# Kernel optimization log

Hardware: AMD Instinct MI355X
Metric: run time of the kernel (lower is better)

The kernel has to match this reference:

```python
import jax, jax.numpy as jnp
import numpy as np

N_NODES = 20000
N_EDGES = 200000
D_IN = 32      # nf_input_dim
D_H = 32       # nf_hide_dim
D_OUT = 8      # nf_output_dim
E_DIM = 16     # edge_dim


def setup_inputs() -> dict:
    key = jax.random.key(0)
    ks = jax.random.split(key, 20)
    s = 0.1
    inp = {
        "x": jax.random.normal(ks[0], (N_NODES, D_IN), jnp.float32),
        "edge_attr": jax.random.normal(ks[1], (N_EDGES, E_DIM), jnp.float32),
        "edge_index": jax.random.randint(ks[2], (2, N_EDGES), 0, N_NODES, jnp.int32),
    }
    # layer 0: edge MLP (E_DIM->E_DIM->D_IN*D_H), root [D_IN,D_H], bias [D_H]
    inp["w1_0"] = jax.random.normal(ks[3], (E_DIM, E_DIM), jnp.float32) * s
    inp["b1_0"] = jnp.zeros((E_DIM,), jnp.float32)
    inp["w2_0"] = jax.random.normal(ks[4], (E_DIM, D_IN * D_H), jnp.float32) * s
    inp["b2_0"] = jnp.zeros((D_IN * D_H,), jnp.float32)
    inp["root_0"] = jax.random.normal(ks[5], (D_IN, D_H), jnp.float32) * s
    inp["bias_0"] = jnp.zeros((D_H,), jnp.float32)
    # layer 1: edge MLP (E_DIM->E_DIM->D_H*D_H), root [D_H,D_H], bias [D_H]
    inp["w1_1"] = jax.random.normal(ks[6], (E_DIM, E_DIM), jnp.float32) * s
    inp["b1_1"] = jnp.zeros((E_DIM,), jnp.float32)
    inp["w2_1"] = jax.random.normal(ks[7], (E_DIM, D_H * D_H), jnp.float32) * s
    inp["b2_1"] = jnp.zeros((D_H * D_H,), jnp.float32)
    inp["root_1"] = jax.random.normal(ks[8], (D_H, D_H), jnp.float32) * s
    inp["bias_1"] = jnp.zeros((D_H,), jnp.float32)
    # classifier
    inp["cls_w"] = jax.random.normal(ks[9], (D_H, D_OUT), jnp.float32) * s
    inp["cls_b"] = jnp.zeros((D_OUT,), jnp.float32)
    return inp


def _nnconv(x, edge_attr, src, dst, inv_count, w1, b1, w2, b2, root, bias, din, dout, n):
    # edge network: Linear -> ELU -> Linear producing per-edge weight matrix [E, din, dout]
    h = jax.nn.elu(edge_attr @ w1 + b1)
    theta = (h @ w2 + b2).reshape(-1, din, dout)
    # gather source features, per-edge matvec, scatter-mean into dst
    msg = jnp.einsum("ei,eio->eo", x[src], theta)          # [E, dout]
    agg = jax.ops.segment_sum(msg, dst, num_segments=n) * inv_count[:, None]
    return agg + x @ root + bias                            # root weight + bias (PyG defaults)


def reference(x, edge_attr, edge_index,
              w1_0, b1_0, w2_0, b2_0, root_0, bias_0,
              w1_1, b1_1, w2_1, b2_1, root_1, bias_1,
              cls_w, cls_b):
    n = x.shape[0]
    src, dst = edge_index[0], edge_index[1]
    deg = jax.ops.segment_sum(jnp.ones(src.shape[0], x.dtype), dst, num_segments=n)
    inv_count = 1.0 / jnp.maximum(deg, 1.0)
    h = jax.nn.elu(_nnconv(x, edge_attr, src, dst, inv_count,
                           w1_0, b1_0, w2_0, b2_0, root_0, bias_0, D_IN, D_H, n))
    h = jax.nn.elu(_nnconv(h, edge_attr, src, dst, inv_count,
                           w1_1, b1_1, w2_1, b2_1, root_1, bias_1, D_H, D_H, n))
    # dropout is identity in eval mode
    return h @ cls_w + cls_b
```

## Files before the change

### kernel.cpp

```cpp
#include <hip/hip_runtime.h>
#include <hip/hip_bf16.h>
#include <math.h>

#define N_NODES 20000
#define N_EDGES 200000
#define D_H 32
#define E_DIM 16
#define CAP 40
#define NJOBS1 (N_EDGES / 16)
#define GBASE1 ((NJOBS1 + 7) / 8)
#define ABASE (N_NODES / 4)
#define W2S_SHORTS (17 * 2 * 64 * 8)
#define PREP_SHORTS (W2S_SHORTS + 512)
#define XPAIRS (N_NODES * 16)
#define EAPAIRS (N_EDGES * 8)
#define IB2 1563

typedef __attribute__((ext_vector_type(8))) short bf16x8;
typedef __attribute__((ext_vector_type(4))) float f32x4;

__device__ __forceinline__ float elu_f(float v) { return v > 0.f ? v : expm1f(v); }
__device__ __forceinline__ short f2bf(float f) {
    union { __hip_bfloat16 h; short s; } u;
    u.h = __float2bfloat16(f);
    return u.s;
}
__device__ __forceinline__ float bf2f(__hip_bfloat16 h) { return __bfloat162float(h); }
__device__ __forceinline__ unsigned pack2(float lo, float hi) {
    return (unsigned)(unsigned short)f2bf(lo) | ((unsigned)(unsigned short)f2bf(hi) << 16);
}

__global__ __launch_bounds__(256)
void init_kernel(const float* __restrict__ w2_0, const float* __restrict__ b2_0,
                 const float* __restrict__ w1_0, const float* __restrict__ b1_0,
                 const float* __restrict__ w2_1, const float* __restrict__ b2_1,
                 const float* __restrict__ w1_1, const float* __restrict__ b1_1,
                 const float* __restrict__ x, const float* __restrict__ ea,
                 int* __restrict__ cnt, short* __restrict__ prep,
                 unsigned* __restrict__ xbf, unsigned* __restrict__ eabf)
{
    const int gid = blockIdx.x * 256 + threadIdx.x;
    const int nth = IB2 * 256;
    if (gid < N_NODES) cnt[gid] = 0;
    if (gid < 2 * PREP_SHORTS) {
        int layer = gid >= PREP_SHORTS ? 1 : 0;
        int r = gid - layer * PREP_SHORTS;
        const float* w2 = layer ? w2_1 : w2_0;
        const float* b2 = layer ? b2_1 : b2_0;
        const float* w1 = layer ? w1_1 : w1_0;
        const float* b1 = layer ? b1_1 : b1_0;
        float v;
        if (r < W2S_SHORTS) {
            int j = r & 7, l = (r >> 3) & 63, ct = (r >> 9) & 1, kk = r >> 10;
            int ii = (l >> 4) * 8 + j;
            int o = ct * 16 + (l & 15);
            v = (kk < 16) ? w2[kk * 1024 + ii * 32 + o] : b2[ii * 32 + o];
        } else {
            int q = r - W2S_SHORTS;
            int j = q & 7, l = q >> 3;
            int m = l & 15, k = (l >> 4) * 8 + j;
            v = (k < 16) ? w1[k * 16 + m] : (k == 16 ? b1[m] : 0.f);
        }
        prep[gid] = f2bf(v);
    }
    for (int i = gid; i < XPAIRS; i += nth) {
        const float2 p = *(const float2*)(x + (size_t)i * 2);
        xbf[i] = pack2(p.x, p.y);
    }
    for (int i = gid; i < EAPAIRS; i += nth) {
        const float2 p = *(const float2*)(ea + (size_t)i * 2);
        eabf[i] = pack2(p.x, p.y);
    }
}

__global__ __launch_bounds__(256)
void hist_kernel(const int* __restrict__ dst, int* __restrict__ cnt, int* __restrict__ ord) {
    int e = blockIdx.x * 256 + threadIdx.x;
    if (e < N_EDGES) ord[e] = atomicAdd(&cnt[dst[e]], 1);
}

__global__ __launch_bounds__(1024)
void scan_kernel(const int* __restrict__ cnt, int* __restrict__ rowptr) {
    __shared__ int part[1024];
    const int t = threadIdx.x;
    const int base = t * 20;
    int loc[20];
    int sum = 0;
    #pragma unroll
    for (int j = 0; j < 20; ++j) {
        int idx = base + j;
        int v = (idx < N_NODES) ? cnt[idx] : 0;
        loc[j] = v;
        sum += v;
    }
    part[t] = sum;
    __syncthreads();
    for (int off = 1; off < 1024; off <<= 1) {
        int v = (t >= off) ? part[t - off] : 0;
        __syncthreads();
        part[t] += v;
        __syncthreads();
    }
    int run = part[t] - sum;
    #pragma unroll
    for (int j = 0; j < 20; ++j) {
        int idx = base + j;
        if (idx < N_NODES) { rowptr[idx] = run; run += loc[j]; }
    }
    if (t == 0) rowptr[N_NODES] = N_EDGES;
}

template<int MODE>
__global__ __launch_bounds__(512)
void edge_kernel(const short* __restrict__ xbf,
                 const short* __restrict__ eabf,
                 const int* __restrict__ src,
                 const int* __restrict__ dst,
                 int* __restrict__ cnt,
                 int* __restrict__ pebuf,
                 const int* __restrict__ ord,
                 const int* __restrict__ rowptr,
                 const short* __restrict__ prepL,
                 __hip_bfloat16* __restrict__ msg)
{
    __shared__ __align__(16) short w2s[PREP_SHORTS];

    const int t = threadIdx.x;
    for (int i = t; i < PREP_SHORTS / 8; i += 512)
        ((int4*)w2s)[i] = ((const int4*)prepL)[i];
    __syncthreads();

    const int lane = t & 63;
    const int wave = t >> 6;
    const int job = blockIdx.x * 8 + wave;
    if (job >= NJOBS1) return;
    const int eloc = lane & 15;
    const int kg = lane >> 4;

    const int e0 = job * 16 + eloc;

    int pe0;
    if (MODE == 0) {
        int p0_ = 0;
        if (kg == 0) {
            const int d0 = dst[e0];
            p0_ = d0 * CAP + atomicAdd(&cnt[d0], 1);
            pebuf[e0] = p0_;
        }
        pe0 = __shfl(p0_, eloc);
    } else if (MODE == 1) {
        pe0 = pebuf[e0];
    } else {
        pe0 = rowptr[dst[e0]] + ord[e0];
    }

    const int sn0 = src[e0];

    bf16x8 xf0 = *(const bf16x8*)(xbf + (size_t)sn0 * 32 + kg * 8);

    bf16x8 ea0 = {0,0,0,0,0,0,0,0};
    if (kg < 2) {
        ea0 = *(const bf16x8*)(eabf + (size_t)e0 * E_DIM + kg * 8);
    } else if (kg == 2) {
        ea0[0] = f2bf(1.0f);
    }

    const f32x4 zero4 = {0.f, 0.f, 0.f, 0.f};

    bf16x8 w1f = *(const bf16x8*)&w2s[W2S_SHORTS + lane * 8];
    f32x4 hd0 = __builtin_amdgcn_mfma_f32_16x16x32_bf16(w1f, ea0, zero4, 0, 0, 0);
    float hv0[4];
    #pragma unroll
    for (int r = 0; r < 4; ++r) hv0[r] = elu_f(hd0[r]);

    float m00[4]={0,0,0,0}, m01[4]={0,0,0,0};
    #pragma unroll
    for (int kk = 0; kk < 17; ++kk) {
        bf16x8 a0 = *(const bf16x8*)&w2s[(kk * 2 + 0) * 512 + lane * 8];
        bf16x8 a1 = *(const bf16x8*)&w2s[(kk * 2 + 1) * 512 + lane * 8];
        float h0;
        if (kk < 16) {
            h0 = __shfl(hv0[kk & 3], (kk >> 2) * 16 + eloc);
        } else {
            h0 = 1.0f;
        }
        f32x4 d00 = __builtin_amdgcn_mfma_f32_16x16x32_bf16(a0, xf0, zero4, 0, 0, 0);
        f32x4 d01 = __builtin_amdgcn_mfma_f32_16x16x32_bf16(a1, xf0, zero4, 0, 0, 0);
        #pragma unroll
        for (int r = 0; r < 4; ++r) {
            m00[r] += h0 * d00[r];
            m01[r] += h0 * d01[r];
        }
    }

    short* mp0 = (short*)(msg + (size_t)pe0 * D_H);
    short q00[4] = { f2bf(m00[0]), f2bf(m00[1]), f2bf(m00[2]), f2bf(m00[3]) };
    short q01[4] = { f2bf(m01[0]), f2bf(m01[1]), f2bf(m01[2]), f2bf(m01[3]) };
    *(int2*)(mp0 + kg * 4)      = *(int2*)q00;
    *(int2*)(mp0 + 16 + kg * 4) = *(int2*)q01;
}

template<bool LAST, bool PADDED>
__global__ __launch_bounds__(256)
void agg_kernel(const void* __restrict__ xin_,
                const __hip_bfloat16* __restrict__ msg,
                const int* __restrict__ rowptr,
                const int* __restrict__ cnt,
                const float* __restrict__ root,
                const float* __restrict__ bias,
                const float* __restrict__ cls_w,
                const float* __restrict__ cls_b,
                __hip_bfloat16* __restrict__ hout,
                float* __restrict__ out)
{
    __shared__ float root_s[32 * 32];
    __shared__ float bias_s[32];
    __shared__ float h2_s[4][33];
    const int t = threadIdx.x;
    for (int i = t; i < 1024; i += 256) root_s[i] = root[i];
    if (t < 32) bias_s[t] = bias[t];
    __syncthreads();

    const int lane = t & 63;
    const int wave = t >> 6;
    const int o = lane & 31;
    const int half = lane >> 5;
    const int n = blockIdx.x * 4 + wave;

    int start, end;
    if (PADDED) { start = n * CAP; end = start + cnt[n]; }
    else        { start = rowptr[n]; end = rowptr[n + 1]; }

    float s = 0.f;
    int j = start + half;
    for (; j + 6 < end; j += 8) {
        float v0 = bf2f(msg[(size_t)(j    ) * D_H + o]);
        float v1 = bf2f(msg[(size_t)(j + 2) * D_H + o]);
        float v2 = bf2f(msg[(size_t)(j + 4) * D_H + o]);
        float v3 = bf2f(msg[(size_t)(j + 6) * D_H + o]);
        s += (v0 + v1) + (v2 + v3);
    }
    for (; j < end; j += 2)
        s += bf2f(msg[(size_t)j * D_H + o]);
    s += __shfl_xor(s, 32);

    float acc = s * (1.f / fmaxf((float)(end - start), 1.f)) + bias_s[o];
    const float xv = LAST ? bf2f(((const __hip_bfloat16*)xin_)[(size_t)n * 32 + o])
                          : ((const float*)xin_)[(size_t)n * 32 + o];
    #pragma unroll
    for (int i = 0; i < 32; ++i)
        acc += __shfl(xv, half * 32 + i) * root_s[i * 32 + o];
    acc = elu_f(acc);

    if (!LAST) {
        if (half == 0) hout[(size_t)n * 32 + o] = __float2bfloat16(acc);
    } else {
        if (half == 0) h2_s[wave][o] = acc;
        __syncthreads();
        if (t < 32) {
            const int nn = t >> 3, jj = t & 7;
            float a = cls_b[jj];
            #pragma unroll
            for (int i = 0; i < 32; ++i) a += h2_s[nn][i] * cls_w[i * 8 + jj];
            out[(size_t)(blockIdx.x * 4 + nn) * 8 + jj] = a;
        }
    }
}

extern "C" void kernel_launch(void* const* d_in, const int* in_sizes, int n_in,
                              void* d_out, int out_size, void* d_ws, size_t ws_size,
                              hipStream_t stream)
{
    const float* x          = (const float*)d_in[0];
    const float* edge_attr  = (const float*)d_in[1];
    const int*   edge_index = (const int*)d_in[2];
    const float* w1_0 = (const float*)d_in[3];
    const float* b1_0 = (const float*)d_in[4];
    const float* w2_0 = (const float*)d_in[5];
    const float* b2_0 = (const float*)d_in[6];
    const float* root_0 = (const float*)d_in[7];
    const float* bias_0 = (const float*)d_in[8];
    const float* w1_1 = (const float*)d_in[9];
    const float* b1_1 = (const float*)d_in[10];
    const float* w2_1 = (const float*)d_in[11];
    const float* b2_1 = (const float*)d_in[12];
    const float* root_1 = (const float*)d_in[13];
    const float* bias_1 = (const float*)d_in[14];
    const float* cls_w = (const float*)d_in[15];
    const float* cls_b = (const float*)d_in[16];

    const int* src = edge_index;
    const int* dst = edge_index + N_EDGES;

    const int EB = (N_EDGES + 255) / 256;

    size_t need = 0;
    size_t o_cnt = need;  need += (size_t)N_NODES * 4;
    size_t o_pe  = need;  need += (size_t)N_EDGES * 4;
    size_t o_prep= (need + 15) & ~(size_t)15; need = o_prep + (size_t)2 * PREP_SHORTS * 2;
    size_t o_xbf = (need + 15) & ~(size_t)15; need = o_xbf + (size_t)N_NODES * 32 * 2;
    size_t o_ea  = (need + 15) & ~(size_t)15; need = o_ea  + (size_t)N_EDGES * 16 * 2;
    size_t o_msg = (need + 63) & ~(size_t)63; need = o_msg + (size_t)N_NODES * CAP * D_H * 2;
    size_t o_hb  = (need + 15) & ~(size_t)15; need = o_hb + (size_t)N_NODES * D_H * 2;

    char* ws = (char*)d_ws;

    if (ws_size >= need) {
        int* cnt = (int*)(ws + o_cnt);
        int* pe  = (int*)(ws + o_pe);
        short* prep = (short*)(ws + o_prep);
        unsigned* xbf  = (unsigned*)(ws + o_xbf);
        unsigned* eabf = (unsigned*)(ws + o_ea);
        __hip_bfloat16* msg  = (__hip_bfloat16*)(ws + o_msg);
        __hip_bfloat16* hbuf = (__hip_bfloat16*)(ws + o_hb);

        init_kernel<<<IB2, 256, 0, stream>>>(w2_0, b2_0, w1_0, b1_0,
                                             w2_1, b2_1, w1_1, b1_1,
                                             x, edge_attr, cnt, prep, xbf, eabf);
        edge_kernel<0><<<GBASE1, 512, 0, stream>>>((const short*)xbf, (const short*)eabf,
                                                   src, dst, cnt, pe, nullptr, nullptr,
                                                   prep, msg);
        agg_kernel<false, true><<<ABASE, 256, 0, stream>>>(x, msg, nullptr, cnt,
                                                           root_0, bias_0, nullptr, nullptr,
                                                           hbuf, nullptr);
        edge_kernel<1><<<GBASE1, 512, 0, stream>>>((const short*)hbuf, (const short*)eabf,
                                                   src, dst, nullptr, pe, nullptr, nullptr,
                                                   prep + PREP_SHORTS, msg);
        agg_kernel<true, true><<<ABASE, 256, 0, stream>>>(hbuf, msg, nullptr, cnt,
                                                          root_1, bias_1, cls_w, cls_b,
                                                          nullptr, (float*)d_out);
    } else {
        size_t f = 0;
        int* cnt    = (int*)ws;                 f += (size_t)N_NODES * 4;
        int* rowptr = (int*)(ws + f);           f += (size_t)(N_NODES + 1) * 4;
        int* ord    = (int*)(ws + f);           f += (size_t)N_EDGES * 4;
        f = (f + 15) & ~(size_t)15;
        short* prep = (short*)(ws + f);         f += (size_t)2 * PREP_SHORTS * 2;
        f = (f + 15) & ~(size_t)15;
        unsigned* xbf = (unsigned*)(ws + f);    f += (size_t)N_NODES * 32 * 2;
        f = (f + 15) & ~(size_t)15;
        unsigned* eabf = (unsigned*)(ws + f);   f += (size_t)N_EDGES * 16 * 2;
        f = (f + 63) & ~(size_t)63;
        __hip_bfloat16* msg = (__hip_bfloat16*)(ws + f); f += (size_t)N_EDGES * D_H * 2;
        f = (f + 15) & ~(size_t)15;
        __hip_bfloat16* hbuf = (__hip_bfloat16*)(ws + f);

        init_kernel<<<IB2, 256, 0, stream>>>(w2_0, b2_0, w1_0, b1_0,
                                             w2_1, b2_1, w1_1, b1_1,
                                             x, edge_attr, cnt, prep, xbf, eabf);
        hist_kernel<<<EB, 256, 0, stream>>>(dst, cnt, ord);
        scan_kernel<<<1, 1024, 0, stream>>>(cnt, rowptr);

        edge_kernel<2><<<GBASE1, 512, 0, stream>>>((const short*)xbf, (const short*)eabf,
                                                   src, dst, nullptr, nullptr, ord, rowptr,
                                                   prep, msg);
        agg_kernel<false, false><<<ABASE, 256, 0, stream>>>(x, msg, rowptr, nullptr,
                                                            root_0, bias_0, nullptr, nullptr,
                                                            hbuf, nullptr);
        edge_kernel<2><<<GBASE1, 512, 0, stream>>>((const short*)hbuf, (const short*)eabf,
                                                   src, dst, nullptr, nullptr, ord, rowptr,
                                                   prep + PREP_SHORTS, msg);
        agg_kernel<true, false><<<ABASE, 256, 0, stream>>>(hbuf, msg, rowptr, nullptr,
                                                           root_1, bias_1, cls_w, cls_b,
                                                           nullptr, (float*)d_out);
    }
}
```

Before: 80.17 us.

## Fuse edge message and node aggregation into one dst-sorted layer kernel

```diff
diff --git a/kernel.cpp b/kernel.cpp
--- a/kernel.cpp
+++ b/kernel.cpp
@@ -7,9 +7,8 @@
 #define D_H 32
 #define E_DIM 16
 #define CAP 40
-#define NJOBS1 (N_EDGES / 16)
-#define GBASE1 ((NJOBS1 + 7) / 8)
-#define ABASE (N_NODES / 4)
+#define NPB 16
+#define LGRID (N_NODES / NPB)
 #define W2S_SHORTS (17 * 2 * 64 * 8)
 #define PREP_SHORTS (W2S_SHORTS + 512)
 #define XPAIRS (N_NODES * 16)
@@ -74,195 +73,149 @@
 }
 
 __global__ __launch_bounds__(256)
-void hist_kernel(const int* __restrict__ dst, int* __restrict__ cnt, int* __restrict__ ord) {
+void fill_kernel(const int* __restrict__ dst, int* __restrict__ cnt, int* __restrict__ elist) {
     int e = blockIdx.x * 256 + threadIdx.x;
-    if (e < N_EDGES) ord[e] = atomicAdd(&cnt[dst[e]], 1);
-}
-
-__global__ __launch_bounds__(1024)
-void scan_kernel(const int* __restrict__ cnt, int* __restrict__ rowptr) {
-    __shared__ int part[1024];
-    const int t = threadIdx.x;
-    const int base = t * 20;
-    int loc[20];
-    int sum = 0;
-    #pragma unroll
-    for (int j = 0; j < 20; ++j) {
-        int idx = base + j;
-        int v = (idx < N_NODES) ? cnt[idx] : 0;
-        loc[j] = v;
-        sum += v;
-    }
-    part[t] = sum;
-    __syncthreads();
-    for (int off = 1; off < 1024; off <<= 1) {
-        int v = (t >= off) ? part[t - off] : 0;
-        __syncthreads();
-        part[t] += v;
-        __syncthreads();
-    }
-    int run = part[t] - sum;
-    #pragma unroll
-    for (int j = 0; j < 20; ++j) {
-        int idx = base + j;
-        if (idx < N_NODES) { rowptr[idx] = run; run += loc[j]; }
-    }
-    if (t == 0) rowptr[N_NODES] = N_EDGES;
-}
-
-template<int MODE>
+    if (e < N_EDGES) {
+        int d = dst[e];
+        int r = atomicAdd(&cnt[d], 1);
+        elist[d * CAP + r] = e;
+    }
+}
+
+template<bool LAST>
 __global__ __launch_bounds__(512)
-void edge_kernel(const short* __restrict__ xbf,
-                 const short* __restrict__ eabf,
-                 const int* __restrict__ src,
-                 const int* __restrict__ dst,
-                 int* __restrict__ cnt,
-                 int* __restrict__ pebuf,
-                 const int* __restrict__ ord,
-                 const int* __restrict__ rowptr,
-                 const short* __restrict__ prepL,
-                 __hip_bfloat16* __restrict__ msg)
+void layer_kernel(const short* __restrict__ xin,
+                  const short* __restrict__ eabf,
+                  const int* __restrict__ src,
+                  const int* __restrict__ elist,
+                  const int* __restrict__ cnt,
+                  const short* __restrict__ prepL,
+                  const float* __restrict__ root,
+                  const float* __restrict__ bias,
+                  const float* __restrict__ cls_w,
+                  const float* __restrict__ cls_b,
+                  __hip_bfloat16* __restrict__ hout,
+                  float* __restrict__ out)
 {
     __shared__ __align__(16) short w2s[PREP_SHORTS];
+    __shared__ float root_s[1024];
+    __shared__ float bias_s[32];
+    __shared__ float acc[NPB + 1][32];
+    __shared__ int   list[NPB * CAP];
+    __shared__ int   off_s[NPB + 1];
+    __shared__ float h2_s[LAST ? NPB : 1][33];
 
     const int t = threadIdx.x;
+    const int nb = blockIdx.x * NPB;
+
     for (int i = t; i < PREP_SHORTS / 8; i += 512)
         ((int4*)w2s)[i] = ((const int4*)prepL)[i];
+    for (int i = t; i < 1024; i += 512) root_s[i] = root[i];
+    if (t < 32) bias_s[t] = bias[t];
+    for (int i = t; i < (NPB + 1) * 32; i += 512) ((float*)acc)[i] = 0.f;
+    if (t == 0) {
+        int run = 0;
+        #pragma unroll
+        for (int ln = 0; ln < NPB; ++ln) { off_s[ln] = run; run += cnt[nb + ln]; }
+        off_s[NPB] = run;
+    }
+    __syncthreads();
+
+    {
+        const int ln = t >> 5;
+        const int j0 = t & 31;
+        const int c = cnt[nb + ln];
+        const int base = off_s[ln];
+        for (int j = j0; j < c; j += 32)
+            list[base + j] = (ln << 20) | elist[(nb + ln) * CAP + j];
+    }
     __syncthreads();
 
     const int lane = t & 63;
     const int wave = t >> 6;
-    const int job = blockIdx.x * 8 + wave;
-    if (job >= NJOBS1) return;
     const int eloc = lane & 15;
     const int kg = lane >> 4;
-
-    const int e0 = job * 16 + eloc;
-
-    int pe0;
-    if (MODE == 0) {
-        int p0_ = 0;
-        if (kg == 0) {
-            const int d0 = dst[e0];
-            p0_ = d0 * CAP + atomicAdd(&cnt[d0], 1);
-            pebuf[e0] = p0_;
-        }
-        pe0 = __shfl(p0_, eloc);
-    } else if (MODE == 1) {
-        pe0 = pebuf[e0];
-    } else {
-        pe0 = rowptr[dst[e0]] + ord[e0];
-    }
-
-    const int sn0 = src[e0];
-
-    bf16x8 xf0 = *(const bf16x8*)(xbf + (size_t)sn0 * 32 + kg * 8);
-
-    bf16x8 ea0 = {0,0,0,0,0,0,0,0};
-    if (kg < 2) {
-        ea0 = *(const bf16x8*)(eabf + (size_t)e0 * E_DIM + kg * 8);
-    } else if (kg == 2) {
-        ea0[0] = f2bf(1.0f);
-    }
-
+    const int total = off_s[NPB];
+    const int ntiles = (total + 15) / 16;
     const f32x4 zero4 = {0.f, 0.f, 0.f, 0.f};
-
-    bf16x8 w1f = *(const bf16x8*)&w2s[W2S_SHORTS + lane * 8];
-    f32x4 hd0 = __builtin_amdgcn_mfma_f32_16x16x32_bf16(w1f, ea0, zero4, 0, 0, 0);
-    float hv0[4];
-    #pragma unroll
-    for (int r = 0; r < 4; ++r) hv0[r] = elu_f(hd0[r]);
-
-    float m00[4]={0,0,0,0}, m01[4]={0,0,0,0};
-    #pragma unroll
-    for (int kk = 0; kk < 17; ++kk) {
-        bf16x8 a0 = *(const bf16x8*)&w2s[(kk * 2 + 0) * 512 + lane * 8];
-        bf16x8 a1 = *(const bf16x8*)&w2s[(kk * 2 + 1) * 512 + lane * 8];
-        float h0;
-        if (kk < 16) {
-            h0 = __shfl(hv0[kk & 3], (kk >> 2) * 16 + eloc);
+    const bf16x8 w1f = *(const bf16x8*)&w2s[W2S_SHORTS + lane * 8];
+
+    for (int tile = wave; tile < ntiles; tile += 8) {
+        const int slot = tile * 16 + eloc;
+        const int packed = (slot < total) ? list[slot] : (NPB << 20);
+        const int ln = packed >> 20;
+        const int e0 = packed & 0xFFFFF;
+
+        const int sn0 = src[e0];
+        const bf16x8 xf0 = *(const bf16x8*)(xin + (size_t)sn0 * 32 + kg * 8);
+
+        bf16x8 ea0 = {0, 0, 0, 0, 0, 0, 0, 0};
+        if (kg < 2) {
+            ea0 = *(const bf16x8*)(eabf + (size_t)e0 * E_DIM + kg * 8);
+        } else if (kg == 2) {
+            ea0[0] = f2bf(1.0f);
+        }
+
+        f32x4 hd0 = __builtin_amdgcn_mfma_f32_16x16x32_bf16(w1f, ea0, zero4, 0, 0, 0);
+        float hv0[4];
+        #pragma unroll
+        for (int r = 0; r < 4; ++r) hv0[r] = elu_f(hd0[r]);
+
+        float m00[4] = {0, 0, 0, 0}, m01[4] = {0, 0, 0, 0};
+        #pragma unroll
+        for (int kk = 0; kk < 17; ++kk) {
+            bf16x8 a0 = *(const bf16x8*)&w2s[(kk * 2 + 0) * 512 + lane * 8];
+            bf16x8 a1 = *(const bf16x8*)&w2s[(kk * 2 + 1) * 512 + lane * 8];
+            float h0;
+            if (kk < 16) {
+                h0 = __shfl(hv0[kk & 3], (kk >> 2) * 16 + eloc);
+            } else {
+                h0 = 1.0f;
+            }
+            f32x4 d00 = __builtin_amdgcn_mfma_f32_16x16x32_bf16(a0, xf0, zero4, 0, 0, 0);
+            f32x4 d01 = __builtin_amdgcn_mfma_f32_16x16x32_bf16(a1, xf0, zero4, 0, 0, 0);
+            #pragma unroll
+            for (int r = 0; r < 4; ++r) {
+                m00[r] += h0 * d00[r];
+                m01[r] += h0 * d01[r];
+            }
+        }
+
+        float* arow = acc[ln];
+        #pragma unroll
+        for (int r = 0; r < 4; ++r) {
+            atomicAdd(&arow[kg * 4 + r],      m00[r]);
+            atomicAdd(&arow[16 + kg * 4 + r], m01[r]);
+        }
+    }
+    __syncthreads();
+
+    {
+        const int half = lane >> 5;
+        const int o = lane & 31;
+        const int ln = wave * 2 + half;
+        const int n = nb + ln;
+        const int c = cnt[n];
+
+        float a = acc[ln][o] * (1.f / fmaxf((float)c, 1.f)) + bias_s[o];
+        const float xv = bf2f(((const __hip_bfloat16*)xin)[(size_t)n * 32 + o]);
+        #pragma unroll
+        for (int i = 0; i < 32; ++i)
+            a += __shfl(xv, half * 32 + i) * root_s[i * 32 + o];
+        a = elu_f(a);
+
+        if (!LAST) {
+            hout[(size_t)n * 32 + o] = __float2bfloat16(a);
         } else {
-            h0 = 1.0f;
-        }
-        f32x4 d00 = __builtin_amdgcn_mfma_f32_16x16x32_bf16(a0, xf0, zero4, 0, 0, 0);
-        f32x4 d01 = __builtin_amdgcn_mfma_f32_16x16x32_bf16(a1, xf0, zero4, 0, 0, 0);
-        #pragma unroll
-        for (int r = 0; r < 4; ++r) {
-            m00[r] += h0 * d00[r];
-            m01[r] += h0 * d01[r];
-        }
-    }
-
-    short* mp0 = (short*)(msg + (size_t)pe0 * D_H);
-    short q00[4] = { f2bf(m00[0]), f2bf(m00[1]), f2bf(m00[2]), f2bf(m00[3]) };
-    short q01[4] = { f2bf(m01[0]), f2bf(m01[1]), f2bf(m01[2]), f2bf(m01[3]) };
-    *(int2*)(mp0 + kg * 4)      = *(int2*)q00;
-    *(int2*)(mp0 + 16 + kg * 4) = *(int2*)q01;
-}
-
-template<bool LAST, bool PADDED>
-__global__ __launch_bounds__(256)
-void agg_kernel(const void* __restrict__ xin_,
-                const __hip_bfloat16* __restrict__ msg,
-                const int* __restrict__ rowptr,
-                const int* __restrict__ cnt,
-                const float* __restrict__ root,
-                const float* __restrict__ bias,
-                const float* __restrict__ cls_w,
-                const float* __restrict__ cls_b,
-                __hip_bfloat16* __restrict__ hout,
-                float* __restrict__ out)
-{
-    __shared__ float root_s[32 * 32];
-    __shared__ float bias_s[32];
-    __shared__ float h2_s[4][33];
-    const int t = threadIdx.x;
-    for (int i = t; i < 1024; i += 256) root_s[i] = root[i];
-    if (t < 32) bias_s[t] = bias[t];
-    __syncthreads();
-
-    const int lane = t & 63;
-    const int wave = t >> 6;
-    const int o = lane & 31;
-    const int half = lane >> 5;
-    const int n = blockIdx.x * 4 + wave;
-
-    int start, end;
-    if (PADDED) { start = n * CAP; end = start + cnt[n]; }
-    else        { start = rowptr[n]; end = rowptr[n + 1]; }
-
-    float s = 0.f;
-    int j = start + half;
-    for (; j + 6 < end; j += 8) {
-        float v0 = bf2f(msg[(size_t)(j    ) * D_H + o]);
-        float v1 = bf2f(msg[(size_t)(j + 2) * D_H + o]);
-        float v2 = bf2f(msg[(size_t)(j + 4) * D_H + o]);
-        float v3 = bf2f(msg[(size_t)(j + 6) * D_H + o]);
-        s += (v0 + v1) + (v2 + v3);
-    }
-    for (; j < end; j += 2)
-        s += bf2f(msg[(size_t)j * D_H + o]);
-    s += __shfl_xor(s, 32);
-
-    float acc = s * (1.f / fmaxf((float)(end - start), 1.f)) + bias_s[o];
-    const float xv = LAST ? bf2f(((const __hip_bfloat16*)xin_)[(size_t)n * 32 + o])
-                          : ((const float*)xin_)[(size_t)n * 32 + o];
-    #pragma unroll
-    for (int i = 0; i < 32; ++i)
-        acc += __shfl(xv, half * 32 + i) * root_s[i * 32 + o];
-    acc = elu_f(acc);
-
-    if (!LAST) {
-        if (half == 0) hout[(size_t)n * 32 + o] = __float2bfloat16(acc);
-    } else {
-        if (half == 0) h2_s[wave][o] = acc;
-        __syncthreads();
-        if (t < 32) {
-            const int nn = t >> 3, jj = t & 7;
-            float a = cls_b[jj];
-            #pragma unroll
-            for (int i = 0; i < 32; ++i) a += h2_s[nn][i] * cls_w[i * 8 + jj];
-            out[(size_t)(blockIdx.x * 4 + nn) * 8 + jj] = a;
+            h2_s[ln][o] = a;
+            __syncthreads();
+            if (t < NPB * 8) {
+                const int nn = t >> 3, jj = t & 7;
+                float s = cls_b[jj];
+                #pragma unroll
+                for (int i = 0; i < 32; ++i) s += h2_s[nn][i] * cls_w[i * 8 + jj];
+                out[(size_t)(nb + nn) * 8 + jj] = s;
+            }
         }
     }
 }
@@ -294,74 +247,28 @@
 
     const int EB = (N_EDGES + 255) / 256;
 
-    size_t need = 0;
-    size_t o_cnt = need;  need += (size_t)N_NODES * 4;
-    size_t o_pe  = need;  need += (size_t)N_EDGES * 4;
-    size_t o_prep= (need + 15) & ~(size_t)15; need = o_prep + (size_t)2 * PREP_SHORTS * 2;
-    size_t o_xbf = (need + 15) & ~(size_t)15; need = o_xbf + (size_t)N_NODES * 32 * 2;
-    size_t o_ea  = (need + 15) & ~(size_t)15; need = o_ea  + (size_t)N_EDGES * 16 * 2;
-    size_t o_msg = (need + 63) & ~(size_t)63; need = o_msg + (size_t)N_NODES * CAP * D_H * 2;
-    size_t o_hb  = (need + 15) & ~(size_t)15; need = o_hb + (size_t)N_NODES * D_H * 2;
-
-    char* ws = (char*)d_ws;
-
-    if (ws_size >= need) {
-        int* cnt = (int*)(ws + o_cnt);
-        int* pe  = (int*)(ws + o_pe);
-        short* prep = (short*)(ws + o_prep);
-        unsigned* xbf  = (unsigned*)(ws + o_xbf);
-        unsigned* eabf = (unsigned*)(ws + o_ea);
-        __hip_bfloat16* msg  = (__hip_bfloat16*)(ws + o_msg);
-        __hip_bfloat16* hbuf = (__hip_bfloat16*)(ws + o_hb);
-
-        init_kernel<<<IB2, 256, 0, stream>>>(w2_0, b2_0, w1_0, b1_0,
-                                             w2_1, b2_1, w1_1, b1_1,
-                                             x, edge_attr, cnt, prep, xbf, eabf);
-        edge_kernel<0><<<GBASE1, 512, 0, stream>>>((const short*)xbf, (const short*)eabf,
-                                                   src, dst, cnt, pe, nullptr, nullptr,
-                                                   prep, msg);
-        agg_kernel<false, true><<<ABASE, 256, 0, stream>>>(x, msg, nullptr, cnt,
-                                                           root_0, bias_0, nullptr, nullptr,
-                                                           hbuf, nullptr);
-        edge_kernel<1><<<GBASE1, 512, 0, stream>>>((const short*)hbuf, (const short*)eabf,
-                                                   src, dst, nullptr, pe, nullptr, nullptr,
-                                                   prep + PREP_SHORTS, msg);
-        agg_kernel<true, true><<<ABASE, 256, 0, stream>>>(hbuf, msg, nullptr, cnt,
-                                                          root_1, bias_1, cls_w, cls_b,
-                                                          nullptr, (float*)d_out);
-    } else {
-        size_t f = 0;
-        int* cnt    = (int*)ws;                 f += (size_t)N_NODES * 4;
-        int* rowptr = (int*)(ws + f);           f += (size_t)(N_NODES + 1) * 4;
-        int* ord    = (int*)(ws + f);           f += (size_t)N_EDGES * 4;
-        f = (f + 15) & ~(size_t)15;
-        short* prep = (short*)(ws + f);         f += (size_t)2 * PREP_SHORTS * 2;
-        f = (f + 15) & ~(size_t)15;
-        unsigned* xbf = (unsigned*)(ws + f);    f += (size_t)N_NODES * 32 * 2;
-        f = (f + 15) & ~(size_t)15;
-        unsigned* eabf = (unsigned*)(ws + f);   f += (size_t)N_EDGES * 16 * 2;
-        f = (f + 63) & ~(size_t)63;
-        __hip_bfloat16* msg = (__hip_bfloat16*)(ws + f); f += (size_t)N_EDGES * D_H * 2;
-        f = (f + 15) & ~(size_t)15;
-        __hip_bfloat16* hbuf = (__hip_bfloat16*)(ws + f);
-
-        init_kernel<<<IB2, 256, 0, stream>>>(w2_0, b2_0, w1_0, b1_0,
-                                             w2_1, b2_1, w1_1, b1_1,
-                                             x, edge_attr, cnt, prep, xbf, eabf);
-        hist_kernel<<<EB, 256, 0, stream>>>(dst, cnt, ord);
-        scan_kernel<<<1, 1024, 0, stream>>>(cnt, rowptr);
-
-        edge_kernel<2><<<GBASE1, 512, 0, stream>>>((const short*)xbf, (const short*)eabf,
-                                                   src, dst, nullptr, nullptr, ord, rowptr,
-                                                   prep, msg);
-        agg_kernel<false, false><<<ABASE, 256, 0, stream>>>(x, msg, rowptr, nullptr,
-                                                            root_0, bias_0, nullptr, nullptr,
-                                                            hbuf, nullptr);
-        edge_kernel<2><<<GBASE1, 512, 0, stream>>>((const short*)hbuf, (const short*)eabf,
-                                                   src, dst, nullptr, nullptr, ord, rowptr,
-                                                   prep + PREP_SHORTS, msg);
-        agg_kernel<true, false><<<ABASE, 256, 0, stream>>>(hbuf, msg, rowptr, nullptr,
-                                                           root_1, bias_1, cls_w, cls_b,
-                                                           nullptr, (float*)d_out);
-    }
-}
+    size_t off = 0;
+    int* cnt = (int*)((char*)d_ws + off);            off += (size_t)N_NODES * 4;
+    int* elist = (int*)((char*)d_ws + off);          off += (size_t)N_NODES * CAP * 4;
+    off = (off + 15) & ~(size_t)15;
+    short* prep = (short*)((char*)d_ws + off);       off += (size_t)2 * PREP_SHORTS * 2;
+    off = (off + 15) & ~(size_t)15;
+    unsigned* xbf = (unsigned*)((char*)d_ws + off);  off += (size_t)N_NODES * 32 * 2;
+    off = (off + 15) & ~(size_t)15;
+    unsigned* eabf = (unsigned*)((char*)d_ws + off); off += (size_t)N_EDGES * 16 * 2;
+    off = (off + 15) & ~(size_t)15;
+    __hip_bfloat16* hbuf = (__hip_bfloat16*)((char*)d_ws + off);
+
+    init_kernel<<<IB2, 256, 0, stream>>>(w2_0, b2_0, w1_0, b1_0,
+                                         w2_1, b2_1, w1_1, b1_1,
+                                         x, edge_attr, cnt, prep, xbf, eabf);
+    fill_kernel<<<EB, 256, 0, stream>>>(dst, cnt, elist);
+    layer_kernel<false><<<LGRID, 512, 0, stream>>>((const short*)xbf, (const short*)eabf,
+                                                   src, elist, cnt, prep,
+                                                   root_0, bias_0, nullptr, nullptr,
+                                                   hbuf, nullptr);
+    layer_kernel<true><<<LGRID, 512, 0, stream>>>((const short*)hbuf, (const short*)eabf,
+                                                  src, elist, cnt, prep + PREP_SHORTS,
+                                                  root_1, bias_1, cls_w, cls_b,
+                                                  nullptr, (float*)d_out);
+}
```

After: 184.2 us. +129.8%, slower.

## Switch edge kernel to 32x32x16 MFMA with 32 edges per wave

Applied to the files above, without the earlier changes.

```diff
diff --git a/kernel.cpp b/kernel.cpp
--- a/kernel.cpp
+++ b/kernel.cpp
@@ -7,17 +7,20 @@
 #define D_H 32
 #define E_DIM 16
 #define CAP 40
-#define NJOBS1 (N_EDGES / 16)
-#define GBASE1 ((NJOBS1 + 7) / 8)
+#define NJOBS32 (N_EDGES / 32)
+#define GB32 ((NJOBS32 + 7) / 8)
 #define ABASE (N_NODES / 4)
 #define W2S_SHORTS (17 * 2 * 64 * 8)
-#define PREP_SHORTS (W2S_SHORTS + 512)
+#define W1_OFF W2S_SHORTS
+#define B1_OFF (W2S_SHORTS + 512)
+#define PREP_SHORTS (W2S_SHORTS + 512 + 32)
 #define XPAIRS (N_NODES * 16)
 #define EAPAIRS (N_EDGES * 8)
 #define IB2 1563
 
 typedef __attribute__((ext_vector_type(8))) short bf16x8;
 typedef __attribute__((ext_vector_type(4))) float f32x4;
+typedef __attribute__((ext_vector_type(16))) float f32x16;
 
 __device__ __forceinline__ float elu_f(float v) { return v > 0.f ? v : expm1f(v); }
 __device__ __forceinline__ short f2bf(float f) {
@@ -26,6 +29,11 @@
     return u.s;
 }
 __device__ __forceinline__ float bf2f(__hip_bfloat16 h) { return __bfloat162float(h); }
+__device__ __forceinline__ float bfbits2f(short s) {
+    union { __hip_bfloat16 h; short s; } u;
+    u.s = s;
+    return __bfloat162float(u.h);
+}
 __device__ __forceinline__ unsigned pack2(float lo, float hi) {
     return (unsigned)(unsigned short)f2bf(lo) | ((unsigned)(unsigned short)f2bf(hi) << 16);
 }
@@ -51,15 +59,18 @@
         const float* b1 = layer ? b1_1 : b1_0;
         float v;
         if (r < W2S_SHORTS) {
-            int j = r & 7, l = (r >> 3) & 63, ct = (r >> 9) & 1, kk = r >> 10;
-            int ii = (l >> 4) * 8 + j;
-            int o = ct * 16 + (l & 15);
-            v = (kk < 16) ? w2[kk * 1024 + ii * 32 + o] : b2[ii * 32 + o];
+            int j = r & 7, l = (r >> 3) & 63, half = (r >> 9) & 1, kk = r >> 10;
+            int i = half * 16 + ((l >> 5) << 3) + j;
+            int o = l & 31;
+            v = (kk < 16) ? w2[kk * 1024 + i * 32 + o] : b2[i * 32 + o];
+        } else if (r < B1_OFF) {
+            int q = r - W1_OFF;
+            int j = q & 7, l = q >> 3;
+            int ko = l & 31, ki = ((l >> 5) << 3) + j;
+            v = (ko < 16) ? w1[ki * 16 + ko] : 0.f;
         } else {
-            int q = r - W2S_SHORTS;
-            int j = q & 7, l = q >> 3;
-            int m = l & 15, k = (l >> 4) * 8 + j;
-            v = (k < 16) ? w1[k * 16 + m] : (k == 16 ? b1[m] : 0.f);
+            int j = r - B1_OFF;
+            v = (j < 16) ? b1[j] : 0.f;
         }
         prep[gid] = f2bf(v);
     }
@@ -133,71 +144,74 @@
     const int lane = t & 63;
     const int wave = t >> 6;
     const int job = blockIdx.x * 8 + wave;
-    if (job >= NJOBS1) return;
-    const int eloc = lane & 15;
-    const int kg = lane >> 4;
-
-    const int e0 = job * 16 + eloc;
-
-    int pe0;
+    if (job >= NJOBS32) return;
+    const int ec = lane & 31;
+    const int hl = lane >> 5;
+
+    const int e = job * 32 + ec;
+
+    int pe;
     if (MODE == 0) {
-        int p0_ = 0;
-        if (kg == 0) {
-            const int d0 = dst[e0];
-            p0_ = d0 * CAP + atomicAdd(&cnt[d0], 1);
-            pebuf[e0] = p0_;
+        int p_ = 0;
+        if (hl == 0) {
+            const int d = dst[e];
+            p_ = d * CAP + atomicAdd(&cnt[d], 1);
+            pebuf[e] = p_;
         }
-        pe0 = __shfl(p0_, eloc);
+        pe = __shfl(p_, ec);
     } else if (MODE == 1) {
-        pe0 = pebuf[e0];
+        pe = pebuf[e];
     } else {
-        pe0 = rowptr[dst[e0]] + ord[e0];
-    }
-
-    const int sn0 = src[e0];
-
-    bf16x8 xf0 = *(const bf16x8*)(xbf + (size_t)sn0 * 32 + kg * 8);
-
-    bf16x8 ea0 = {0,0,0,0,0,0,0,0};
-    if (kg < 2) {
-        ea0 = *(const bf16x8*)(eabf + (size_t)e0 * E_DIM + kg * 8);
-    } else if (kg == 2) {
-        ea0[0] = f2bf(1.0f);
-    }
-
-    const f32x4 zero4 = {0.f, 0.f, 0.f, 0.f};
-
-    bf16x8 w1f = *(const bf16x8*)&w2s[W2S_SHORTS + lane * 8];
-    f32x4 hd0 = __builtin_amdgcn_mfma_f32_16x16x32_bf16(w1f, ea0, zero4, 0, 0, 0);
-    float hv0[4];
-    #pragma unroll
-    for (int r = 0; r < 4; ++r) hv0[r] = elu_f(hd0[r]);
-
-    float m00[4]={0,0,0,0}, m01[4]={0,0,0,0};
+        pe = rowptr[dst[e]] + ord[e];
+    }
+
+    const int sn = src[e];
+
+    const bf16x8 xb0 = *(const bf16x8*)(xbf + (size_t)sn * 32 + hl * 8);
+    const bf16x8 xb1 = *(const bf16x8*)(xbf + (size_t)sn * 32 + 16 + hl * 8);
+
+    const bf16x8 eaB = *(const bf16x8*)(eabf + (size_t)e * E_DIM + hl * 8);
+
+    const f32x16 zero16 = {0.f,0.f,0.f,0.f,0.f,0.f,0.f,0.f,0.f,0.f,0.f,0.f,0.f,0.f,0.f,0.f};
+
+    const bf16x8 w1A = *(const bf16x8*)&w2s[W1_OFF + lane * 8];
+    f32x16 hd = __builtin_amdgcn_mfma_f32_32x32x16_bf16(w1A, eaB, zero16, 0, 0, 0);
+    float hv[8];
+    #pragma unroll
+    for (int r = 0; r < 8; ++r) {
+        const int row = (r & 3) + 8 * (r >> 2) + 4 * hl;
+        hv[r] = elu_f(hd[r] + bfbits2f(w2s[B1_OFF + row]));
+    }
+
+    float mr[16];
+    #pragma unroll
+    for (int r = 0; r < 16; ++r) mr[r] = 0.f;
+
     #pragma unroll
     for (int kk = 0; kk < 17; ++kk) {
-        bf16x8 a0 = *(const bf16x8*)&w2s[(kk * 2 + 0) * 512 + lane * 8];
-        bf16x8 a1 = *(const bf16x8*)&w2s[(kk * 2 + 1) * 512 + lane * 8];
-        float h0;
+        const bf16x8 a0 = *(const bf16x8*)&w2s[((kk * 2 + 0) * 64 + lane) * 8];
+        const bf16x8 a1 = *(const bf16x8*)&w2s[((kk * 2 + 1) * 64 + lane) * 8];
+        f32x16 d = __builtin_amdgcn_mfma_f32_32x32x16_bf16(a0, xb0, zero16, 0, 0, 0);
+        d = __builtin_amdgcn_mfma_f32_32x32x16_bf16(a1, xb1, d, 0, 0, 0);
+        float h;
         if (kk < 16) {
-            h0 = __shfl(hv0[kk & 3], (kk >> 2) * 16 + eloc);
+            const int hlk = (kk >> 2) & 1;
+            const int rk = (kk & 3) | ((kk & 8) >> 1);
+            h = __shfl(hv[rk], hlk * 32 + ec);
         } else {
-            h0 = 1.0f;
+            h = 1.0f;
         }
-        f32x4 d00 = __builtin_amdgcn_mfma_f32_16x16x32_bf16(a0, xf0, zero4, 0, 0, 0);
-        f32x4 d01 = __builtin_amdgcn_mfma_f32_16x16x32_bf16(a1, xf0, zero4, 0, 0, 0);
         #pragma unroll
-        for (int r = 0; r < 4; ++r) {
-            m00[r] += h0 * d00[r];
-            m01[r] += h0 * d01[r];
-        }
-    }
-
-    short* mp0 = (short*)(msg + (size_t)pe0 * D_H);
-    short q00[4] = { f2bf(m00[0]), f2bf(m00[1]), f2bf(m00[2]), f2bf(m00[3]) };
-    short q01[4] = { f2bf(m01[0]), f2bf(m01[1]), f2bf(m01[2]), f2bf(m01[3]) };
-    *(int2*)(mp0 + kg * 4)      = *(int2*)q00;
-    *(int2*)(mp0 + 16 + kg * 4) = *(int2*)q01;
+        for (int r = 0; r < 16; ++r) mr[r] += h * d[r];
+    }
+
+    short* mp = (short*)(msg + (size_t)pe * D_H);
+    #pragma unroll
+    for (int g = 0; g < 4; ++g) {
+        short q[4] = { f2bf(mr[g * 4 + 0]), f2bf(mr[g * 4 + 1]),
+                       f2bf(mr[g * 4 + 2]), f2bf(mr[g * 4 + 3]) };
+        *(int2*)(mp + 8 * g + 4 * hl) = *(int2*)q;
+    }
 }
 
 template<bool LAST, bool PADDED>
@@ -317,15 +331,15 @@
         init_kernel<<<IB2, 256, 0, stream>>>(w2_0, b2_0, w1_0, b1_0,
                                              w2_1, b2_1, w1_1, b1_1,
                                              x, edge_attr, cnt, prep, xbf, eabf);
-        edge_kernel<0><<<GBASE1, 512, 0, stream>>>((const short*)xbf, (const short*)eabf,
-                                                   src, dst, cnt, pe, nullptr, nullptr,
-                                                   prep, msg);
+        edge_kernel<0><<<GB32, 512, 0, stream>>>((const short*)xbf, (const short*)eabf,
+                                                 src, dst, cnt, pe, nullptr, nullptr,
+                                                 prep, msg);
         agg_kernel<false, true><<<ABASE, 256, 0, stream>>>(x, msg, nullptr, cnt,
                                                            root_0, bias_0, nullptr, nullptr,
                                                            hbuf, nullptr);
-        edge_kernel<1><<<GBASE1, 512, 0, stream>>>((const short*)hbuf, (const short*)eabf,
-                                                   src, dst, nullptr, pe, nullptr, nullptr,
-                                                   prep + PREP_SHORTS, msg);
+        edge_kernel<1><<<GB32, 512, 0, stream>>>((const short*)hbuf, (const short*)eabf,
+                                                 src, dst, nullptr, pe, nullptr, nullptr,
+                                                 prep + PREP_SHORTS, msg);
         agg_kernel<true, true><<<ABASE, 256, 0, stream>>>(hbuf, msg, nullptr, cnt,
                                                           root_1, bias_1, cls_w, cls_b,
                                                           nullptr, (float*)d_out);
@@ -351,15 +365,15 @@
         hist_kernel<<<EB, 256, 0, stream>>>(dst, cnt, ord);
         scan_kernel<<<1, 1024, 0, stream>>>(cnt, rowptr);
 
-        edge_kernel<2><<<GBASE1, 512, 0, stream>>>((const short*)xbf, (const short*)eabf,
-                                                   src, dst, nullptr, nullptr, ord, rowptr,
-                                                   prep, msg);
+        edge_kernel<2><<<GB32, 512, 0, stream>>>((const short*)xbf, (const short*)eabf,
+                                                 src, dst, nullptr, nullptr, ord, rowptr,
+                                                 prep, msg);
         agg_kernel<false, false><<<ABASE, 256, 0, stream>>>(x, msg, rowptr, nullptr,
                                                             root_0, bias_0, nullptr, nullptr,
                                                             hbuf, nullptr);
-        edge_kernel<2><<<GBASE1, 512, 0, stream>>>((const short*)hbuf, (const short*)eabf,
-                                                   src, dst, nullptr, nullptr, ord, rowptr,
-                                                   prep + PREP_SHORTS, msg);
+        edge_kernel<2><<<GB32, 512, 0, stream>>>((const short*)hbuf, (const short*)eabf,
+                                                 src, dst, nullptr, nullptr, ord, rowptr,
+                                                 prep + PREP_SHORTS, msg);
         agg_kernel<true, false><<<ABASE, 256, 0, stream>>>(hbuf, msg, rowptr, nullptr,
                                                            root_1, bias_1, cls_w, cls_b,
                                                            nullptr, (float*)d_out);
```

Measured after the change: 81.87 us. +2.1%, slower.
